# Optimization experiments

Measured on AMD Instinct MI355X. Metric: run time of the kernel, lower is better.

Reference implementation:

```python
import jax, jax.numpy as jnp
import numpy as np

B, L, S, E, H = 2, 2048, 2048, 1024, 16
D = E // H


def setup_inputs() -> dict:
    key = jax.random.key(0)
    ks = jax.random.split(key, 16)
    p = 0.02  # small init scale for weights
    return {
        "a": jax.random.normal(ks[0], (B, L, E), jnp.float32),
        "b": jax.random.normal(ks[1], (B, S, E), jnp.float32),
        "Wa_qk": jax.random.normal(ks[2], (E, E), jnp.float32) * p,
        "ba_qk": jax.random.normal(ks[3], (E,), jnp.float32) * p,
        "Wa_v": jax.random.normal(ks[4], (E, E), jnp.float32) * p,
        "ba_v": jax.random.normal(ks[5], (E,), jnp.float32) * p,
        "Wb_qk": jax.random.normal(ks[6], (E, E), jnp.float32) * p,
        "bb_qk": jax.random.normal(ks[7], (E,), jnp.float32) * p,
        "Wb_v": jax.random.normal(ks[8], (E, E), jnp.float32) * p,
        "bb_v": jax.random.normal(ks[9], (E,), jnp.float32) * p,
        "Wa_o": jax.random.normal(ks[10], (E, E), jnp.float32) * p,
        "ba_o": jax.random.normal(ks[11], (E,), jnp.float32) * p,
        "Wb_o": jax.random.normal(ks[12], (E, E), jnp.float32) * p,
        "bb_o": jax.random.normal(ks[13], (E,), jnp.float32) * p,
    }


def _heads(x, n, W, bias):
    # x: [B, N, E] -> projected and split to [B, H, N, D]
    y = x @ W + bias
    return y.reshape(B, n, H, D).transpose(0, 2, 1, 3)


def reference(a, b, Wa_qk, ba_qk, Wa_v, ba_v, Wb_qk, bb_qk, Wb_v, bb_v,
              Wa_o, ba_o, Wb_o, bb_o):
    aq = _heads(a, L, Wa_qk, ba_qk)   # [B,H,L,D]
    av = _heads(a, L, Wa_v, ba_v)     # [B,H,L,D]
    bq = _heads(b, S, Wb_qk, bb_qk)   # [B,H,S,D]
    bv = _heads(b, S, Wb_v, bb_v)     # [B,H,S,D]

    scale = 1.0 / jnp.sqrt(jnp.float32(D))
    # Shared score matrix [B,H,L,S]
    scores = jnp.einsum('bhld,bhsd->bhls', aq, bq) * scale
    # Dual softmax: row-wise (over S) and column-wise (over L)
    wa = jax.nn.softmax(scores, axis=-1)                    # [B,H,L,S]
    wb = jax.nn.softmax(scores, axis=-2).transpose(0, 1, 3, 2)  # [B,H,S,L]

    a_ctx = jnp.einsum('bhls,bhsd->bhld', wa, bv)  # [B,H,L,D]
    b_ctx = jnp.einsum('bhsl,bhld->bhsd', wb, av)  # [B,H,S,D]

    a_out = a_ctx.transpose(0, 2, 1, 3).reshape(B, L, E) @ Wa_o + ba_o
    b_out = b_ctx.transpose(0, 2, 1, 3).reshape(B, S, E) @ Wb_o + bb_o
    return (a_out, b_out)
```

## Files before the change

kernel.cpp:

```cpp
#include <hip/hip_runtime.h>
#include <hip/hip_bf16.h>
#include <stdint.h>

typedef unsigned short u16;
typedef unsigned int u32;
typedef __attribute__((ext_vector_type(8))) short bf16x8;
typedef __attribute__((ext_vector_type(4))) float f32x4;

typedef __attribute__((address_space(3))) void lds_void;
typedef const __attribute__((address_space(1))) void gbl_void;

#define SIDE 4194304u
#define BHSTR 131072u

static __device__ __forceinline__ u16 f2bf(float f) {
  union { __hip_bfloat16 b; u16 u; } cv;
  cv.b = __float2bfloat16(f);
  return cv.u;
}
static __device__ __forceinline__ float bf2f(u16 u) {
  union { __hip_bfloat16 b; u16 u; } cv;
  cv.u = u;
  return __bfloat162float(cv.b);
}

__global__ __launch_bounds__(256) void k_cvt_in(const float* __restrict__ a,
                                                const float* __restrict__ b,
                                                u16* __restrict__ dst) {
  int z = blockIdx.y;
  const float* src = z ? b : a;
  size_t i = ((size_t)blockIdx.x * 256 + threadIdx.x) * 8;
  float4 x0 = *(const float4*)(src + i);
  float4 x1 = *(const float4*)(src + i + 4);
  u16 t[8] = {f2bf(x0.x), f2bf(x0.y), f2bf(x0.z), f2bf(x0.w),
              f2bf(x1.x), f2bf(x1.y), f2bf(x1.z), f2bf(x1.w)};
  *(uint4*)(dst + (size_t)z * SIDE + i) = *(uint4*)t;
}

__global__ __launch_bounds__(256) void k_cvt_bias(
    const float* s0, const float* s1, const float* s2, const float* s3,
    const float* s4, const float* s5, u16* __restrict__ dst) {
  const float* srcs[6] = {s0, s1, s2, s3, s4, s5};
  int z = blockIdx.y;
  int i = blockIdx.x * 256 + threadIdx.x;
  float sc = (z == 0) ? 0.125f : 1.0f;
  dst[z * 1024 + i] = f2bf(srcs[z][i] * sc);
}

__global__ __launch_bounds__(256) void k_transpose_w(
    const float* a0, const float* a1, const float* a2, const float* a3,
    const float* a4, const float* a5,
    u16* d0, u16* d1, u16* d2, u16* d3, u16* d4, u16* d5) {
  __shared__ u16 tile[64][72];
  const float* srcs[6] = {a0, a1, a2, a3, a4, a5};
  u16* dsts[6] = {d0, d1, d2, d3, d4, d5};
  int z = blockIdx.z;
  float sc = (z == 0) ? 0.125f : 1.0f;
  const float* src = srcs[z] + (size_t)(blockIdx.y * 64) * 1024 + blockIdx.x * 64;
  int t = threadIdx.x;
  int row = t >> 2, c4 = t & 3;
#pragma unroll
  for (int p = 0; p < 2; ++p) {
    int col = c4 * 8 + p * 32;
    const float* sf = src + (size_t)row * 1024 + col;
    float4 x0 = *(const float4*)sf;
    float4 x1 = *(const float4*)(sf + 4);
    u16 tmp[8] = {f2bf(x0.x * sc), f2bf(x0.y * sc), f2bf(x0.z * sc), f2bf(x0.w * sc),
                  f2bf(x1.x * sc), f2bf(x1.y * sc), f2bf(x1.z * sc), f2bf(x1.w * sc)};
    *(uint4*)(&tile[row][col]) = *(uint4*)tmp;
  }
  __syncthreads();
  u16* dst = dsts[z] + (size_t)(blockIdx.x * 64) * 1024 + blockIdx.y * 64;
#pragma unroll
  for (int p = 0; p < 2; ++p) {
    int col = c4 * 8 + p * 32;
    u16 tmp[8];
#pragma unroll
    for (int i = 0; i < 8; ++i) tmp[i] = tile[col + i][row];
    *(uint4*)(dst + (size_t)row * 1024 + col) = *(uint4*)tmp;
  }
}

__global__ __launch_bounds__(256) void k_gemm_qkv(
    const u16* __restrict__ Aall, const u16* __restrict__ WtA,
    const u16* __restrict__ WtB, const u16* __restrict__ bias,
    u16* __restrict__ qkbuf, u16* __restrict__ vbuf) {
  __shared__ u16 Sh[8192];
  u16* As = Sh;
  u16* Bs = Sh + 4096;
  int tid = threadIdx.x;
  int wave = tid >> 6, lane = tid & 63;
  int quad = lane >> 4, lrow = lane & 15;
  int wr = wave >> 1, wc = wave & 1;
  int z = blockIdx.z;
  int m0 = blockIdx.y * 128, n0 = blockIdx.x * 128;
  const u16* A = Aall + (size_t)z * SIDE;
  const u16* Wt = z ? WtB : WtA;
  const u16* bi = bias + (size_t)z * 2048;

  f32x4 acc[4][4] = {};
  int srow = 32 * wave + (lane >> 2);
  int scol = (lane & 3) * 8;
  const u16* gA = A + (size_t)(m0 + srow) * 1024 + scol;
  const u16* gB = Wt + (size_t)(n0 + srow) * 1024 + scol;
  u16* lA = &As[(32 * wave) * 32];
  u16* lB = &Bs[(32 * wave) * 32];

  for (int k0 = 0; k0 < 1024; k0 += 32) {
    __syncthreads();
#pragma unroll
    for (int j = 0; j < 2; ++j) {
      __builtin_amdgcn_global_load_lds((gbl_void*)(gA + (size_t)(16 * j) * 1024 + k0),
                                       (lds_void*)(lA + 16 * j * 32), 16, 0, 0);
      __builtin_amdgcn_global_load_lds((gbl_void*)(gB + (size_t)(16 * j) * 1024 + k0),
                                       (lds_void*)(lB + 16 * j * 32), 16, 0, 0);
    }
    __syncthreads();
    bf16x8 af[4], bfr[4];
#pragma unroll
    for (int i = 0; i < 4; ++i)
      af[i] = *(const bf16x8*)&As[(64 * wr + 16 * i + lrow) * 32 + 8 * quad];
#pragma unroll
    for (int j = 0; j < 4; ++j)
      bfr[j] = *(const bf16x8*)&Bs[(64 * wc + 16 * j + lrow) * 32 + 8 * quad];
#pragma unroll
    for (int i = 0; i < 4; ++i)
#pragma unroll
      for (int j = 0; j < 4; ++j)
        acc[i][j] = __builtin_amdgcn_mfma_f32_16x16x32_bf16(af[i], bfr[j], acc[i][j], 0, 0, 0);
  }

  float bv[4];
#pragma unroll
  for (int j = 0; j < 4; ++j) bv[j] = bf2f(bi[n0 + 64 * wc + 16 * j + lrow]);

  int x = blockIdx.x;
  bool isv = (x >= 8);
  int h = (isv ? 2 * (x - 8) : 2 * x) + wc;
  u16* dst = (isv ? vbuf : qkbuf) + (size_t)z * SIDE;
  u16* lw = Sh + wave * 1216;

  __syncthreads();
#pragma unroll
  for (int i = 0; i < 4; ++i) {
#pragma unroll
    for (int j = 0; j < 4; ++j)
#pragma unroll
      for (int r = 0; r < 4; ++r)
        lw[(4 * quad + r) * 76 + 16 * j + lrow] = f2bf(acc[i][j][r] + bv[j]);
    asm volatile("s_waitcnt lgkmcnt(0)" ::: "memory");
    int row = lane >> 2, cg = (lane & 3) * 16;
    int rg = m0 + 64 * wr + 16 * i + row;
    int bb = rg >> 11, rl = rg & 2047;
    u16* dr = dst + (size_t)(bb * 16 + h) * BHSTR + (size_t)rl * 64 + cg;
    uint2 w0 = *(const uint2*)&lw[row * 76 + cg];
    uint2 w1 = *(const uint2*)&lw[row * 76 + cg + 4];
    uint2 w2 = *(const uint2*)&lw[row * 76 + cg + 8];
    uint2 w3 = *(const uint2*)&lw[row * 76 + cg + 12];
    uint4 o0 = {w0.x, w0.y, w1.x, w1.y};
    uint4 o1 = {w2.x, w2.y, w3.x, w3.y};
    *(uint4*)dr = o0;
    *(uint4*)(dr + 8) = o1;
    asm volatile("s_waitcnt lgkmcnt(0)" ::: "memory");
  }
}

__global__ __launch_bounds__(256) void k_transpose_v(const u16* __restrict__ v,
                                                     u16* __restrict__ vt) {
  __shared__ u16 tile[64][72];
  int sbh = blockIdx.y;
  int n0 = blockIdx.x * 64;
  const u16* src = v + (size_t)sbh * BHSTR + (size_t)n0 * 64;
  u16* dst = vt + (size_t)sbh * BHSTR + n0;
  int t = threadIdx.x;
  int row = t >> 2, c4 = t & 3;
#pragma unroll
  for (int p = 0; p < 2; ++p) {
    int col = c4 * 8 + p * 32;
    uint4 q = *(const uint4*)(src + (size_t)row * 64 + col);
    *(uint4*)(&tile[row][col]) = q;
  }
  __syncthreads();
#pragma unroll
  for (int p = 0; p < 2; ++p) {
    int col = c4 * 8 + p * 32;
    u16 tmp[8];
#pragma unroll
    for (int i = 0; i < 8; ++i) tmp[i] = tile[col + i][row];
    *(uint4*)(dst + (size_t)row * 2048 + col) = *(uint4*)tmp;
  }
}

__global__ __launch_bounds__(256) void k_attn(
    const u16* __restrict__ qk, const u16* __restrict__ vt,
    u16* __restrict__ ctx) {
  __shared__ u16 Ks[2 * 4096];
  __shared__ u16 Vs[2 * 4096];
  __shared__ u16 Ps[128 * 64];
  int tid = threadIdx.x;
  int wave = tid >> 6, lane = tid & 63;
  int quad = lane >> 4, lrow = lane & 15;
  int z = blockIdx.z, bh = blockIdx.x;
  int l0 = blockIdx.y * 128;
  const u16* Qb = qk + (size_t)z * SIDE + (size_t)bh * BHSTR + (size_t)l0 * 64;
  const u16* Kb = qk + (size_t)(1 - z) * SIDE + (size_t)bh * BHSTR;
  const u16* Vtb = vt + (size_t)(1 - z) * SIDE + (size_t)bh * BHSTR;

#pragma unroll
  for (int p = 0; p < 4; ++p) {
    int G0 = wave * 256 + p * 64;
    int G = G0 + lane;
    int row = G >> 3, c = G & 7;
    __builtin_amdgcn_global_load_lds((gbl_void*)(Qb + (size_t)row * 64 + ((c ^ (row & 7)) * 8)),
                                     (lds_void*)(Ps + G0 * 8), 16, 0, 0);
  }
#pragma unroll
  for (int p = 0; p < 2; ++p) {
    int G0 = p * 256 + wave * 64;
    int G = G0 + lane;
    int row = G >> 3, c = G & 7;
    int sw = (c ^ (row & 7)) * 8;
    __builtin_amdgcn_global_load_lds((gbl_void*)(Kb + (size_t)row * 64 + sw),
                                     (lds_void*)(Ks + G0 * 8), 16, 0, 0);
    __builtin_amdgcn_global_load_lds((gbl_void*)(Vtb + (size_t)row * 2048 + sw),
                                     (lds_void*)(Vs + G0 * 8), 16, 0, 0);
  }

  bf16x8 qf[2][2];
  f32x4 cacc[2][4] = {};
  float rsum[2] = {0.f, 0.f};
  int e = 2 * (lrow & 7);

  for (int it = 0; it < 32; ++it) {
    __syncthreads();
    if (it == 0) {
#pragma unroll
      for (int rt = 0; rt < 2; ++rt) {
        int lq = 32 * wave + 16 * rt + lrow;
        qf[rt][0] = *(const bf16x8*)&Ps[(lq * 8 + (quad ^ (lq & 7))) * 8];
        qf[rt][1] = *(const bf16x8*)&Ps[(lq * 8 + ((quad + 4) ^ (lq & 7))) * 8];
      }
    }
    int prty = it & 1;
    if (it + 1 < 32) {
      int s1 = (it + 1) << 6;
      int nb = (1 - prty) * 4096;
#pragma unroll
      for (int p = 0; p < 2; ++p) {
        int G0 = p * 256 + wave * 64;
        int G = G0 + lane;
        int row = G >> 3, c = G & 7;
        int sw = (c ^ (row & 7)) * 8;
        __builtin_amdgcn_global_load_lds((gbl_void*)(Kb + (size_t)(s1 + row) * 64 + sw),
                                         (lds_void*)(Ks + nb + G0 * 8), 16, 0, 0);
        __builtin_amdgcn_global_load_lds((gbl_void*)(Vtb + (size_t)row * 2048 + s1 + sw),
                                         (lds_void*)(Vs + nb + G0 * 8), 16, 0, 0);
      }
    }
    const u16* KsC = Ks + prty * 4096;
    const u16* VsC = Vs + prty * 4096;
#pragma unroll
    for (int j = 0; j < 4; ++j) {
      int kr = 16 * j + lrow;
      bf16x8 kf0 = *(const bf16x8*)&KsC[(kr * 8 + (quad ^ (kr & 7))) * 8];
      bf16x8 kf1 = *(const bf16x8*)&KsC[(kr * 8 + ((quad + 4) ^ (kr & 7))) * 8];
#pragma unroll
      for (int rt = 0; rt < 2; ++rt) {
        f32x4 s = {};
        s = __builtin_amdgcn_mfma_f32_16x16x32_bf16(kf0, qf[rt][0], s, 0, 0, 0);
        s = __builtin_amdgcn_mfma_f32_16x16x32_bf16(kf1, qf[rt][1], s, 0, 0, 0);
        float e0 = __expf(s[0]), e1 = __expf(s[1]);
        float e2 = __expf(s[2]), e3 = __expf(s[3]);
        rsum[rt] += (e0 + e1) + (e2 + e3);
        uint2 pk;
        pk.x = ((u32)f2bf(e1) << 16) | (u32)f2bf(e0);
        pk.y = ((u32)f2bf(e3) << 16) | (u32)f2bf(e2);
        *(uint2*)&Ps[(32 * wave + 16 * rt + lrow) * 64 + ((4 * j + quad) ^ e) * 4] = pk;
      }
    }
    asm volatile("s_waitcnt lgkmcnt(0)" ::: "memory");
    bf16x8 pf[2][2];
#pragma unroll
    for (int rt = 0; rt < 2; ++rt) {
      const u16* pr = &Ps[(32 * wave + 16 * rt + lrow) * 64];
      pf[rt][0] = *(const bf16x8*)&pr[((2 * quad) ^ e) * 4];
      pf[rt][1] = *(const bf16x8*)&pr[((2 * quad + 8) ^ e) * 4];
    }
#pragma unroll
    for (int j = 0; j < 4; ++j) {
      int vr = 16 * j + lrow;
      bf16x8 vf0 = *(const bf16x8*)&VsC[(vr * 8 + (quad ^ (vr & 7))) * 8];
      bf16x8 vf1 = *(const bf16x8*)&VsC[(vr * 8 + ((quad + 4) ^ (vr & 7))) * 8];
#pragma unroll
      for (int rt = 0; rt < 2; ++rt) {
        cacc[rt][j] = __builtin_amdgcn_mfma_f32_16x16x32_bf16(pf[rt][0], vf0, cacc[rt][j], 0, 0, 0);
        cacc[rt][j] = __builtin_amdgcn_mfma_f32_16x16x32_bf16(pf[rt][1], vf1, cacc[rt][j], 0, 0, 0);
      }
    }
  }

  float rinv[2][4];
#pragma unroll
  for (int rt = 0; rt < 2; ++rt) {
    float v = rsum[rt];
    v += __shfl_xor(v, 16);
    v += __shfl_xor(v, 32);
    float rv = 1.0f / v;
#pragma unroll
    for (int r = 0; r < 4; ++r)
      rinv[rt][r] = __shfl(rv, 20 * quad + r);
  }

  int bb = bh >> 4, h = bh & 15;
  u16* Ob = ctx + (size_t)z * SIDE + (size_t)(bb * 2048 + l0) * 1024 + h * 64;
#pragma unroll
  for (int rt = 0; rt < 2; ++rt)
#pragma unroll
    for (int r = 0; r < 4; ++r) {
      int l = 32 * wave + 16 * rt + 4 * quad + r;
#pragma unroll
      for (int j = 0; j < 4; ++j)
        Ob[(size_t)l * 1024 + 16 * j + lrow] = f2bf(cacc[rt][j][r] * rinv[rt][r]);
    }
}

__global__ __launch_bounds__(256) void k_gemm_o(
    const u16* __restrict__ ctx, const u16* __restrict__ WtO,
    const u16* __restrict__ bias, float* __restrict__ out) {
  __shared__ u16 As[128 * 32];
  __shared__ u16 Bs[128 * 32];
  int tid = threadIdx.x;
  int wave = tid >> 6, lane = tid & 63;
  int quad = lane >> 4, lrow = lane & 15;
  int wr = wave >> 1, wc = wave & 1;
  int z = blockIdx.z;
  int m0 = blockIdx.y * 128, n0 = blockIdx.x * 128;
  const u16* A = ctx + (size_t)z * SIDE;
  const u16* Wt = WtO + (size_t)z * 1048576;
  const u16* bi = bias + (size_t)z * 1024;
  float* C = out + (size_t)z * SIDE;

  f32x4 acc[4][4] = {};
  int srow = 32 * wave + (lane >> 2);
  int scol = (lane & 3) * 8;
  const u16* gA = A + (size_t)(m0 + srow) * 1024 + scol;
  const u16* gB = Wt + (size_t)(n0 + srow) * 1024 + scol;
  u16* lA = &As[(32 * wave) * 32];
  u16* lB = &Bs[(32 * wave) * 32];

  for (int k0 = 0; k0 < 1024; k0 += 32) {
    __syncthreads();
#pragma unroll
    for (int j = 0; j < 2; ++j) {
      __builtin_amdgcn_global_load_lds((gbl_void*)(gA + (size_t)(16 * j) * 1024 + k0),
                                       (lds_void*)(lA + 16 * j * 32), 16, 0, 0);
      __builtin_amdgcn_global_load_lds((gbl_void*)(gB + (size_t)(16 * j) * 1024 + k0),
                                       (lds_void*)(lB + 16 * j * 32), 16, 0, 0);
    }
    __syncthreads();
    bf16x8 af[4], bfr[4];
#pragma unroll
    for (int i = 0; i < 4; ++i)
      af[i] = *(const bf16x8*)&As[(64 * wr + 16 * i + lrow) * 32 + 8 * quad];
#pragma unroll
    for (int j = 0; j < 4; ++j)
      bfr[j] = *(const bf16x8*)&Bs[(64 * wc + 16 * j + lrow) * 32 + 8 * quad];
#pragma unroll
    for (int i = 0; i < 4; ++i)
#pragma unroll
      for (int j = 0; j < 4; ++j)
        acc[i][j] = __builtin_amdgcn_mfma_f32_16x16x32_bf16(af[i], bfr[j], acc[i][j], 0, 0, 0);
  }

  float bv[4];
#pragma unroll
  for (int j = 0; j < 4; ++j) bv[j] = bf2f(bi[n0 + 64 * wc + 16 * j + lrow]);
#pragma unroll
  for (int i = 0; i < 4; ++i) {
    int row = m0 + 64 * wr + 16 * i + 4 * quad;
#pragma unroll
    for (int j = 0; j < 4; ++j) {
      int col = n0 + 64 * wc + 16 * j + lrow;
#pragma unroll
      for (int r = 0; r < 4; ++r)
        C[(size_t)(row + r) * 1024 + col] = acc[i][j][r] + bv[j];
    }
  }
}

extern "C" void kernel_launch(void* const* d_in, const int* in_sizes, int n_in,
                              void* d_out, int out_size, void* d_ws, size_t ws_size,
                              hipStream_t stream) {
  (void)in_sizes; (void)n_in; (void)out_size; (void)ws_size;
  const size_t M1 = 1048576u;
  u16* ws = (u16*)d_ws;
  u16* wtA   = ws;
  u16* wtB   = ws + 2 * M1;
  u16* wtO   = ws + 4 * M1;
  u16* biasQ = ws + 6 * M1;
  u16* biasO = ws + 6 * M1 + 4096;
  u16* ab    = ws + 7 * M1;
  u16* vt    = ab;
  u16* qkbuf = ws + 15 * M1;
  u16* vbuf  = ws + 23 * M1;
  u16* ctx   = vbuf;

  dim3 blk(256);
  k_cvt_in<<<dim3(2048, 2), blk, 0, stream>>>((const float*)d_in[0],
                                              (const float*)d_in[1], ab);
  k_cvt_bias<<<dim3(4, 6), blk, 0, stream>>>(
      (const float*)d_in[3], (const float*)d_in[5], (const float*)d_in[7],
      (const float*)d_in[9], (const float*)d_in[11], (const float*)d_in[13], biasQ);
  k_transpose_w<<<dim3(16, 16, 6), blk, 0, stream>>>(
      (const float*)d_in[2], (const float*)d_in[4], (const float*)d_in[6],
      (const float*)d_in[8], (const float*)d_in[10], (const float*)d_in[12],
      wtA, wtA + M1, wtB, wtB + M1, wtO, wtO + M1);
  k_gemm_qkv<<<dim3(16, 32, 2), blk, 0, stream>>>(ab, wtA, wtB, biasQ, qkbuf, vbuf);
  k_transpose_v<<<dim3(32, 64), blk, 0, stream>>>(vbuf, vt);
  k_attn<<<dim3(32, 16, 2), blk, 0, stream>>>(qkbuf, vt, ctx);
  k_gemm_o<<<dim3(8, 32, 2), blk, 0, stream>>>(ctx, wtO, biasO, (float*)d_out);
}
```

Baseline: 315.1 us.

## Merge prep kernels, use exp2 with folded log2e scale, and split attention P tile

Three preprocessing launches (input conversion, bias conversion, weight transpose) become one kernel that branches on block index, and the float-to-bf16 conversion now packs two values per instruction. The Q scale gains a log2(e) factor so attention can use exp2 directly instead of expf. Q fragments are read straight from global memory into registers instead of going through LDS. The P tile is processed in two 32-column halves, which halves the shared buffer and interleaves the exp/store work with the PV MFMAs. The aim is to cut launch overhead, transcendental cost and LDS footprint, at the cost of a more divergent prep kernel and an extra sync point per half-tile.

After: 356.9 us. 13.3% more time.

```diff
diff --git a/kernel.cpp b/kernel.cpp
--- a/kernel.cpp
+++ b/kernel.cpp
@@ -12,6 +12,7 @@
 
 #define SIDE 4194304u
 #define BHSTR 131072u
+#define QK_SCALE 0.18033688011112042f
 
 static __device__ __forceinline__ u16 f2bf(float f) {
   union { __hip_bfloat16 b; u16 u; } cv;
@@ -23,61 +24,70 @@
   cv.u = u;
   return __bfloat162float(cv.b);
 }
-
-__global__ __launch_bounds__(256) void k_cvt_in(const float* __restrict__ a,
-                                                const float* __restrict__ b,
-                                                u16* __restrict__ dst) {
-  int z = blockIdx.y;
-  const float* src = z ? b : a;
-  size_t i = ((size_t)blockIdx.x * 256 + threadIdx.x) * 8;
-  float4 x0 = *(const float4*)(src + i);
-  float4 x1 = *(const float4*)(src + i + 4);
-  u16 t[8] = {f2bf(x0.x), f2bf(x0.y), f2bf(x0.z), f2bf(x0.w),
-              f2bf(x1.x), f2bf(x1.y), f2bf(x1.z), f2bf(x1.w)};
-  *(uint4*)(dst + (size_t)z * SIDE + i) = *(uint4*)t;
-}
-
-__global__ __launch_bounds__(256) void k_cvt_bias(
-    const float* s0, const float* s1, const float* s2, const float* s3,
-    const float* s4, const float* s5, u16* __restrict__ dst) {
-  const float* srcs[6] = {s0, s1, s2, s3, s4, s5};
-  int z = blockIdx.y;
-  int i = blockIdx.x * 256 + threadIdx.x;
-  float sc = (z == 0) ? 0.125f : 1.0f;
-  dst[z * 1024 + i] = f2bf(srcs[z][i] * sc);
-}
-
-__global__ __launch_bounds__(256) void k_transpose_w(
-    const float* a0, const float* a1, const float* a2, const float* a3,
-    const float* a4, const float* a5,
-    u16* d0, u16* d1, u16* d2, u16* d3, u16* d4, u16* d5) {
+static __device__ __forceinline__ u32 pk2bf(float x, float y) {
+  float2 f = {x, y};
+  union { __hip_bfloat162 b; u32 u; } cv;
+  cv.b = __float22bfloat162_rn(f);
+  return cv.u;
+}
+
+__global__ __launch_bounds__(256) void k_prep(
+    const float* __restrict__ a, const float* __restrict__ b, u16* __restrict__ ab,
+    const float* w0, const float* w1, const float* w2, const float* w3,
+    const float* w4, const float* w5, u16* __restrict__ wt,
+    const float* b0, const float* b1, const float* b2, const float* b3,
+    const float* b4, const float* b5, u16* __restrict__ bias) {
   __shared__ u16 tile[64][72];
-  const float* srcs[6] = {a0, a1, a2, a3, a4, a5};
-  u16* dsts[6] = {d0, d1, d2, d3, d4, d5};
-  int z = blockIdx.z;
-  float sc = (z == 0) ? 0.125f : 1.0f;
-  const float* src = srcs[z] + (size_t)(blockIdx.y * 64) * 1024 + blockIdx.x * 64;
-  int t = threadIdx.x;
-  int row = t >> 2, c4 = t & 3;
-#pragma unroll
-  for (int p = 0; p < 2; ++p) {
-    int col = c4 * 8 + p * 32;
-    const float* sf = src + (size_t)row * 1024 + col;
-    float4 x0 = *(const float4*)sf;
-    float4 x1 = *(const float4*)(sf + 4);
-    u16 tmp[8] = {f2bf(x0.x * sc), f2bf(x0.y * sc), f2bf(x0.z * sc), f2bf(x0.w * sc),
-                  f2bf(x1.x * sc), f2bf(x1.y * sc), f2bf(x1.z * sc), f2bf(x1.w * sc)};
-    *(uint4*)(&tile[row][col]) = *(uint4*)tmp;
-  }
-  __syncthreads();
-  u16* dst = dsts[z] + (size_t)(blockIdx.x * 64) * 1024 + blockIdx.y * 64;
-#pragma unroll
-  for (int p = 0; p < 2; ++p) {
-    int col = c4 * 8 + p * 32;
-    u16 tmp[8];
-#pragma unroll
-    for (int i = 0; i < 8; ++i) tmp[i] = tile[col + i][row];
-    *(uint4*)(dst + (size_t)row * 1024 + col) = *(uint4*)tmp;
+  int bid = blockIdx.x;
+  int tid = threadIdx.x;
+  if (bid < 4096) {
+    int z = bid >> 11;
+    const float* src = z ? b : a;
+    size_t i = ((size_t)(bid & 2047) * 256 + tid) * 8;
+    float4 x0 = *(const float4*)(src + i);
+    float4 x1 = *(const float4*)(src + i + 4);
+    uint4 o = {pk2bf(x0.x, x0.y), pk2bf(x0.z, x0.w),
+               pk2bf(x1.x, x1.y), pk2bf(x1.z, x1.w)};
+    *(uint4*)(ab + (size_t)z * SIDE + i) = o;
+    return;
+  }
+  if (bid < 4120) {
+    const float* srcs[6] = {b0, b1, b2, b3, b4, b5};
+    int t = bid - 4096;
+    int z = t >> 2;
+    int i = (t & 3) * 256 + tid;
+    float sc = (z == 0) ? QK_SCALE : 1.0f;
+    bias[z * 1024 + i] = f2bf(srcs[z][i] * sc);
+    return;
+  }
+  {
+    const float* srcs[6] = {w0, w1, w2, w3, w4, w5};
+    int t = bid - 4120;
+    int z = t >> 8;
+    int bx = t & 15, by = (t >> 4) & 15;
+    float sc = (z == 0) ? QK_SCALE : 1.0f;
+    const float* src = srcs[z] + (size_t)(by * 64) * 1024 + bx * 64;
+    int row = tid >> 2, c4 = tid & 3;
+#pragma unroll
+    for (int p = 0; p < 2; ++p) {
+      int col = c4 * 8 + p * 32;
+      const float* sf = src + (size_t)row * 1024 + col;
+      float4 x0 = *(const float4*)sf;
+      float4 x1 = *(const float4*)(sf + 4);
+      uint4 o = {pk2bf(x0.x * sc, x0.y * sc), pk2bf(x0.z * sc, x0.w * sc),
+                 pk2bf(x1.x * sc, x1.y * sc), pk2bf(x1.z * sc, x1.w * sc)};
+      *(uint4*)(&tile[row][col]) = o;
+    }
+    __syncthreads();
+    u16* dst = wt + (size_t)z * 1048576u + (size_t)(bx * 64) * 1024 + by * 64;
+#pragma unroll
+    for (int p = 0; p < 2; ++p) {
+      int col = c4 * 8 + p * 32;
+      u16 tmp[8];
+#pragma unroll
+      for (int i = 0; i < 8; ++i) tmp[i] = tile[col + i][row];
+      *(uint4*)(dst + (size_t)row * 1024 + col) = *(uint4*)tmp;
+    }
   }
 }
 
@@ -196,7 +206,7 @@
     u16* __restrict__ ctx) {
   __shared__ u16 Ks[2 * 4096];
   __shared__ u16 Vs[2 * 4096];
-  __shared__ u16 Ps[128 * 64];
+  __shared__ u16 Ps[128 * 32];
   int tid = threadIdx.x;
   int wave = tid >> 6, lane = tid & 63;
   int quad = lane >> 4, lrow = lane & 15;
@@ -206,14 +216,14 @@
   const u16* Kb = qk + (size_t)(1 - z) * SIDE + (size_t)bh * BHSTR;
   const u16* Vtb = vt + (size_t)(1 - z) * SIDE + (size_t)bh * BHSTR;
 
-#pragma unroll
-  for (int p = 0; p < 4; ++p) {
-    int G0 = wave * 256 + p * 64;
-    int G = G0 + lane;
-    int row = G >> 3, c = G & 7;
-    __builtin_amdgcn_global_load_lds((gbl_void*)(Qb + (size_t)row * 64 + ((c ^ (row & 7)) * 8)),
-                                     (lds_void*)(Ps + G0 * 8), 16, 0, 0);
-  }
+  bf16x8 qf[2][2];
+#pragma unroll
+  for (int rt = 0; rt < 2; ++rt)
+#pragma unroll
+    for (int d = 0; d < 2; ++d)
+      qf[rt][d] = *(const bf16x8*)(Qb + (size_t)(32 * wave + 16 * rt + lrow) * 64 +
+                                   32 * d + 8 * quad);
+
 #pragma unroll
   for (int p = 0; p < 2; ++p) {
     int G0 = p * 256 + wave * 64;
@@ -226,21 +236,12 @@
                                      (lds_void*)(Vs + G0 * 8), 16, 0, 0);
   }
 
-  bf16x8 qf[2][2];
   f32x4 cacc[2][4] = {};
   float rsum[2] = {0.f, 0.f};
-  int e = 2 * (lrow & 7);
+  int key = (lrow >> 1) & 7;
 
   for (int it = 0; it < 32; ++it) {
     __syncthreads();
-    if (it == 0) {
-#pragma unroll
-      for (int rt = 0; rt < 2; ++rt) {
-        int lq = 32 * wave + 16 * rt + lrow;
-        qf[rt][0] = *(const bf16x8*)&Ps[(lq * 8 + (quad ^ (lq & 7))) * 8];
-        qf[rt][1] = *(const bf16x8*)&Ps[(lq * 8 + ((quad + 4) ^ (lq & 7))) * 8];
-      }
-    }
     int prty = it & 1;
     if (it + 1 < 32) {
       int s1 = (it + 1) << 6;
@@ -260,41 +261,46 @@
     const u16* KsC = Ks + prty * 4096;
     const u16* VsC = Vs + prty * 4096;
 #pragma unroll
-    for (int j = 0; j < 4; ++j) {
-      int kr = 16 * j + lrow;
-      bf16x8 kf0 = *(const bf16x8*)&KsC[(kr * 8 + (quad ^ (kr & 7))) * 8];
-      bf16x8 kf1 = *(const bf16x8*)&KsC[(kr * 8 + ((quad + 4) ^ (kr & 7))) * 8];
+    for (int h = 0; h < 2; ++h) {
+#pragma unroll
+      for (int jj = 0; jj < 2; ++jj) {
+        int j = 2 * h + jj;
+        int kr = 16 * j + lrow;
+        bf16x8 kf0 = *(const bf16x8*)&KsC[(kr * 8 + (quad ^ (kr & 7))) * 8];
+        bf16x8 kf1 = *(const bf16x8*)&KsC[(kr * 8 + ((quad + 4) ^ (kr & 7))) * 8];
+#pragma unroll
+        for (int rt = 0; rt < 2; ++rt) {
+          f32x4 s = {};
+          s = __builtin_amdgcn_mfma_f32_16x16x32_bf16(kf0, qf[rt][0], s, 0, 0, 0);
+          s = __builtin_amdgcn_mfma_f32_16x16x32_bf16(kf1, qf[rt][1], s, 0, 0, 0);
+          float e0 = __builtin_exp2f(s[0]);
+          float e1 = __builtin_exp2f(s[1]);
+          float e2 = __builtin_exp2f(s[2]);
+          float e3 = __builtin_exp2f(s[3]);
+          rsum[rt] += (e0 + e1) + (e2 + e3);
+          uint2 pk = {pk2bf(e0, e1), pk2bf(e2, e3)};
+          int slot = (4 * jj + quad) ^ key;
+          *(uint2*)&Ps[(32 * wave + 16 * rt + lrow) * 32 + slot * 4] = pk;
+        }
+      }
+      asm volatile("s_waitcnt lgkmcnt(0)" ::: "memory");
+      bf16x8 pf[2];
 #pragma unroll
       for (int rt = 0; rt < 2; ++rt) {
-        f32x4 s = {};
-        s = __builtin_amdgcn_mfma_f32_16x16x32_bf16(kf0, qf[rt][0], s, 0, 0, 0);
-        s = __builtin_amdgcn_mfma_f32_16x16x32_bf16(kf1, qf[rt][1], s, 0, 0, 0);
-        float e0 = __expf(s[0]), e1 = __expf(s[1]);
-        float e2 = __expf(s[2]), e3 = __expf(s[3]);
-        rsum[rt] += (e0 + e1) + (e2 + e3);
-        uint2 pk;
-        pk.x = ((u32)f2bf(e1) << 16) | (u32)f2bf(e0);
-        pk.y = ((u32)f2bf(e3) << 16) | (u32)f2bf(e2);
-        *(uint2*)&Ps[(32 * wave + 16 * rt + lrow) * 64 + ((4 * j + quad) ^ e) * 4] = pk;
+        const u16* pr = &Ps[(32 * wave + 16 * rt + lrow) * 32];
+        uint2 lo = *(const uint2*)&pr[((2 * quad) ^ key) * 4];
+        uint2 hi = *(const uint2*)&pr[((2 * quad + 1) ^ key) * 4];
+        union { uint4 u; bf16x8 v; } cv;
+        cv.u = (uint4){lo.x, lo.y, hi.x, hi.y};
+        pf[rt] = cv.v;
       }
-    }
-    asm volatile("s_waitcnt lgkmcnt(0)" ::: "memory");
-    bf16x8 pf[2][2];
-#pragma unroll
-    for (int rt = 0; rt < 2; ++rt) {
-      const u16* pr = &Ps[(32 * wave + 16 * rt + lrow) * 64];
-      pf[rt][0] = *(const bf16x8*)&pr[((2 * quad) ^ e) * 4];
-      pf[rt][1] = *(const bf16x8*)&pr[((2 * quad + 8) ^ e) * 4];
-    }
-#pragma unroll
-    for (int j = 0; j < 4; ++j) {
-      int vr = 16 * j + lrow;
-      bf16x8 vf0 = *(const bf16x8*)&VsC[(vr * 8 + (quad ^ (vr & 7))) * 8];
-      bf16x8 vf1 = *(const bf16x8*)&VsC[(vr * 8 + ((quad + 4) ^ (vr & 7))) * 8];
-#pragma unroll
-      for (int rt = 0; rt < 2; ++rt) {
-        cacc[rt][j] = __builtin_amdgcn_mfma_f32_16x16x32_bf16(pf[rt][0], vf0, cacc[rt][j], 0, 0, 0);
-        cacc[rt][j] = __builtin_amdgcn_mfma_f32_16x16x32_bf16(pf[rt][1], vf1, cacc[rt][j], 0, 0, 0);
+#pragma unroll
+      for (int j2 = 0; j2 < 4; ++j2) {
+        int vr = 16 * j2 + lrow;
+        bf16x8 vfh = *(const bf16x8*)&VsC[(vr * 8 + ((4 * h + quad) ^ (vr & 7))) * 8];
+#pragma unroll
+        for (int rt = 0; rt < 2; ++rt)
+          cacc[rt][j2] = __builtin_amdgcn_mfma_f32_16x16x32_bf16(pf[rt], vfh, cacc[rt][j2], 0, 0, 0);
       }
     }
   }
@@ -311,8 +317,8 @@
       rinv[rt][r] = __shfl(rv, 20 * quad + r);
   }
 
-  int bb = bh >> 4, h = bh & 15;
-  u16* Ob = ctx + (size_t)z * SIDE + (size_t)(bb * 2048 + l0) * 1024 + h * 64;
+  int bb = bh >> 4, hh = bh & 15;
+  u16* Ob = ctx + (size_t)z * SIDE + (size_t)(bb * 2048 + l0) * 1024 + hh * 64;
 #pragma unroll
   for (int rt = 0; rt < 2; ++rt)
 #pragma unroll
@@ -394,9 +400,10 @@
   (void)in_sizes; (void)n_in; (void)out_size; (void)ws_size;
   const size_t M1 = 1048576u;
   u16* ws = (u16*)d_ws;
-  u16* wtA   = ws;
-  u16* wtB   = ws + 2 * M1;
-  u16* wtO   = ws + 4 * M1;
+  u16* wt    = ws;
+  u16* wtA   = wt;
+  u16* wtB   = wt + 2 * M1;
+  u16* wtO   = wt + 4 * M1;
   u16* biasQ = ws + 6 * M1;
   u16* biasO = ws + 6 * M1 + 4096;
   u16* ab    = ws + 7 * M1;
@@ -406,15 +413,12 @@
   u16* ctx   = vbuf;
 
   dim3 blk(256);
-  k_cvt_in<<<dim3(2048, 2), blk, 0, stream>>>((const float*)d_in[0],
-                                              (const float*)d_in[1], ab);
-  k_cvt_bias<<<dim3(4, 6), blk, 0, stream>>>(
+  k_prep<<<dim3(5656), blk, 0, stream>>>(
+      (const float*)d_in[0], (const float*)d_in[1], ab,
+      (const float*)d_in[2], (const float*)d_in[4], (const float*)d_in[6],
+      (const float*)d_in[8], (const float*)d_in[10], (const float*)d_in[12], wt,
       (const float*)d_in[3], (const float*)d_in[5], (const float*)d_in[7],
       (const float*)d_in[9], (const float*)d_in[11], (const float*)d_in[13], biasQ);
-  k_transpose_w<<<dim3(16, 16, 6), blk, 0, stream>>>(
-      (const float*)d_in[2], (const float*)d_in[4], (const float*)d_in[6],
-      (const float*)d_in[8], (const float*)d_in[10], (const float*)d_in[12],
-      wtA, wtA + M1, wtB, wtB + M1, wtO, wtO + M1);
   k_gemm_qkv<<<dim3(16, 32, 2), blk, 0, stream>>>(ab, wtA, wtB, biasQ, qkbuf, vbuf);
   k_transpose_v<<<dim3(32, 64), blk, 0, stream>>>(vbuf, vt);
   k_attn<<<dim3(32, 16, 2), blk, 0, stream>>>(qkbuf, vt, ctx);
```
